# Optimization experiments

Measured on AMD Instinct MI355X. Metric: run time of the kernel, lower is better.

Reference implementation:

```python
import jax, jax.numpy as jnp
import numpy as np

K = 2  # kernel_size


def setup_inputs() -> dict:
    key = jax.random.key(0)
    k1, k2, k3, k4, k5 = jax.random.split(key, 5)
    B, C, H, W_sp = 8, 256, 128, 128
    N = 512                      # number of keypoints
    E = C * K * K                # embed_dim = 1024
    img_feat_highres = jax.random.normal(k1, (B, C, H, W_sp), dtype=jnp.float32)
    W = jax.random.normal(k2, (E, C, K, K), dtype=jnp.float32) * 0.02  # conv weight, OIHW
    b = jax.random.normal(k3, (E,), dtype=jnp.float32) * 0.02          # conv bias
    batch_indices = jnp.broadcast_to(jnp.arange(B, dtype=jnp.int64)[:, None], (B, N))
    pixel_x_id = jax.random.randint(k4, (B, N), 0, H // 2, dtype=jnp.int64)  # low-res ids
    pixel_y_id = jax.random.randint(k5, (B, N), 0, H // 2, dtype=jnp.int64)
    return {
        "img_feat_highres": img_feat_highres,
        "W": W,
        "b": b,
        "batch_indices": batch_indices,
        "pixel_x_id": pixel_x_id,
        "pixel_y_id": pixel_y_id,
    }


def reference(img_feat_highres, W, b, batch_indices, pixel_x_id, pixel_y_id):
    # Dense conv2d, stride 1, padding = K-1 (torch nn.Conv2d semantics)
    patches = jax.lax.conv_general_dilated(
        img_feat_highres, W,
        window_strides=(1, 1),
        padding=((K - 1, K - 1), (K - 1, K - 1)),
        dimension_numbers=("NCHW", "OIHW", "NCHW"),
    ) + b[None, :, None, None]  # (B, E, H+K-1, W+K-1)

    y0 = 2 * pixel_y_id  # (B, N)
    x0 = 2 * pixel_x_id

    def samp(dy, dx):
        # advanced indices at dims 0,2,3 (non-adjacent) -> result (B, N, E)
        return patches[batch_indices, :, y0 + dy, x0 + dx]

    local_feat = jnp.concatenate(
        [samp(0, 0), samp(K, 0), samp(0, K), samp(K, K)], axis=2
    )  # (B, N, 4E)
    return jnp.transpose(local_feat, (0, 2, 1))  # (B, 4E, N)
```

## Files before the change

kernel.cpp:

```cpp
#include <hip/hip_runtime.h>
#include <stdint.h>


typedef __attribute__((ext_vector_type(8))) short bf16x8;
typedef __attribute__((ext_vector_type(4))) float f32x4;

#define GAS(p) ((const __attribute__((address_space(1))) void*)(p))
#define LAS(p) ((__attribute__((address_space(3))) void*)(p))

__device__ __forceinline__ unsigned short f2bf(float f) {
    union { float f; uint32_t u; } x; x.f = f;
    uint32_t u = x.u;
    uint32_t r = (u + 0x7FFFu + ((u >> 16) & 1u)) >> 16;
    return (unsigned short)r;
}

__global__ __launch_bounds__(256)
void prep_kernel(const float* __restrict__ img, const float* __restrict__ Wf,
                 unsigned short* __restrict__ Wq, unsigned short* __restrict__ zp,
                 unsigned short* __restrict__ imgT) {
    __shared__ unsigned short sT[8192];
    const int blk = blockIdx.x;
    const int tid = threadIdx.x;

    if (blk < 512) {
        if (blk == 0 && tid < 32) {
            uint4 z = {0, 0, 0, 0};
            ((uint4*)zp)[tid] = z;
        }
        const int t  = blk * 256 + tid;
        const int et = t >> 15;
        const int r1 = t & 32767;
        const int j  = r1 >> 11;
        const int r2 = r1 & 2047;
        const int h  = r2 >> 10;
        const int r3 = r2 & 1023;
        const int chunk = r3 >> 8;
        const int row   = r3 & 255;
        const int e  = et * 256 + row;
        const int kb = j * 64 + h * 32 + chunk * 8;
        unsigned short v[8];
        #pragma unroll
        for (int kk = 0; kk < 8; ++kk) {
            const int k = kb + kk;
            const int c = k & 255;
            const int p = k >> 8;
            v[kk] = f2bf(Wf[(size_t)e * 1024 + c * 4 + p]);
        }
        *(uint4*)&Wq[(size_t)t * 8] = *(const uint4*)v;
        return;
    }

    const int ib = blk - 512;
    const int cc = ib & 3;
    const int y  = (ib >> 2) & 127;
    const int b  = ib >> 9;
    const int xq = tid & 31;
    const int ch = tid >> 5;
    unsigned int* sU = (unsigned int*)sT;
    const size_t pl = ((size_t)b * 256 + cc * 64) * 16384 + (size_t)y * 128;
    #pragma unroll
    for (int it = 0; it < 4; ++it) {
        const int cp = it * 8 + ch;
        const float4 v0 = *(const float4*)&img[pl + (size_t)(2 * cp)     * 16384 + xq * 4];
        const float4 v1 = *(const float4*)&img[pl + (size_t)(2 * cp + 1) * 16384 + xq * 4];
        const float a0[4] = {v0.x, v0.y, v0.z, v0.w};
        const float a1[4] = {v1.x, v1.y, v1.z, v1.w};
        #pragma unroll
        for (int jj = 0; jj < 4; ++jj) {
            const int x = xq * 4 + jj;
            const unsigned int pk = (unsigned)f2bf(a0[jj]) | ((unsigned)f2bf(a1[jj]) << 16);
            sU[x * 32 + (cp ^ (x & 31))] = pk;
        }
    }
    __syncthreads();
    unsigned short* ob = imgT + (((size_t)b * 128 + y) * 128) * 256 + cc * 64;
    #pragma unroll
    for (int jj = 0; jj < 16; ++jj) {
        const int oo = tid + 256 * jj;
        const int xx = oo >> 5;
        const int c2 = oo & 31;
        const unsigned int pk = sU[xx * 32 + (c2 ^ (xx & 31))];
        *(unsigned int*)&ob[(size_t)xx * 256 + c2 * 2] = pk;
    }
}

__global__ __launch_bounds__(512, 1)
void gemm_kernel(const unsigned short* __restrict__ Wq,
                 const unsigned short* __restrict__ imgT,
                 const unsigned short* __restrict__ zp,
                 const int* __restrict__ bidx,
                 const int* __restrict__ pxid,
                 const int* __restrict__ pyid,
                 const float* __restrict__ bias,
                 float* __restrict__ out)
{
    const int orig = blockIdx.x;
    const int xcd  = orig & 7;
    const int s    = orig >> 3;
    const int gnt  = xcd * 8 + (s >> 2);
    const int et   = s & 3;
    const int e0   = et * 256;
    const int g    = gnt >> 1;
    const int n0   = (gnt & 1) * 256;
    const int b = g >> 2, o = g & 3;

    const int tid  = threadIdx.x;
    const int lane = tid & 63;
    const int wid  = tid >> 6;
    const int wm   = wid >> 2;
    const int wn   = wid & 3;

    __shared__ unsigned short sW[2 * 16384];
    __shared__ unsigned short sA[2 * 16384];

    int ayv[2], axv[2];
    size_t apl[2];
    #pragma unroll
    for (int u = 0; u < 2; ++u) {
        const int row = u * 128 + (tid >> 2);
        const int gi = b * 512 + n0 + row;
        apl[u] = (size_t)bidx[gi] * (128 * 128 * 256);
        ayv[u] = 2 * pyid[gi] - 1 + (o & 1) * 2;
        axv[u] = 2 * pxid[gi] - 1 + (o >> 1) * 2;
    }
    const int aswz = (((tid & 3) ^ ((tid >> 3) & 3))) * 8;
    const unsigned short* wq_base = Wq + (size_t)et * 262144 + tid * 8;

    f32x4 acc[8][4];
    #pragma unroll
    for (int m = 0; m < 8; ++m)
        #pragma unroll
        for (int nf = 0; nf < 4; ++nf) acc[m][nf] = (f32x4){0.f, 0.f, 0.f, 0.f};

    auto stageHalf = [&](int j, int h, int buf) {
        #pragma unroll
        for (int u = 0; u < 2; ++u) {
            const unsigned short* src = wq_base + (size_t)(j * 2 + h) * 8192 + u * 4096;
            __builtin_amdgcn_global_load_lds(GAS(src),
                LAS(&sW[buf * 16384 + h * 8192 + u * 4096 + tid * 8]), 16, 0, 0);
        }
        const int p = j >> 2;
        const int csh = (j & 3) * 64 + h * 32 + aswz;
        #pragma unroll
        for (int u = 0; u < 2; ++u) {
            const int yy = ayv[u] + (p >> 1);
            const int xx = axv[u] + (p & 1);
            const unsigned short* src =
                ((unsigned)yy < 128u && (unsigned)xx < 128u)
                    ? imgT + apl[u] + ((size_t)(yy * 128 + xx)) * 256 + csh
                    : zp + aswz;
            __builtin_amdgcn_global_load_lds(GAS(src),
                LAS(&sA[buf * 16384 + h * 8192 + u * 4096 + tid * 8]), 16, 0, 0);
        }
    };

    stageHalf(0, 0, 0);
    stageHalf(0, 1, 0);

    for (int j = 0; j < 16; ++j) {
        const int buf = j & 1;
        #pragma unroll
        for (int h = 0; h < 2; ++h) {
            if (j == 15 && h == 1) { asm volatile("s_waitcnt vmcnt(0)" ::: "memory"); }
            else                   { asm volatile("s_waitcnt vmcnt(4)" ::: "memory"); }
            __builtin_amdgcn_s_barrier();
            if (j < 15) stageHalf(j + 1, h, buf ^ 1);

            bf16x8 af[8];
            {
                const int chunk = lane >> 4;
                const int rb = wm * 128 + (lane & 15);
                #pragma unroll
                for (int m = 0; m < 8; ++m)
                    af[m] = *(const bf16x8*)&sW[buf * 16384 + h * 8192 + chunk * 2048 + (rb + m * 16) * 8];
            }
            #pragma unroll
            for (int nh = 0; nh < 2; ++nh) {
                bf16x8 bfr[2];
                #pragma unroll
                for (int nn = 0; nn < 2; ++nn) {
                    const int row = wn * 64 + (nh * 2 + nn) * 16 + (lane & 15);
                    const int perm = (lane >> 4) ^ ((row >> 1) & 3);
                    bfr[nn] = *(const bf16x8*)&sA[buf * 16384 + h * 8192 + row * 32 + perm * 8];
                }
                __builtin_amdgcn_s_setprio(1);
                #pragma unroll
                for (int m = 0; m < 8; ++m)
                    #pragma unroll
                    for (int nn = 0; nn < 2; ++nn)
                        acc[m][nh * 2 + nn] = __builtin_amdgcn_mfma_f32_16x16x32_bf16(
                            af[m], bfr[nn], acc[m][nh * 2 + nn], 0, 0, 0);
                __builtin_amdgcn_s_setprio(0);
            }
        }
    }

    #pragma unroll
    for (int m = 0; m < 8; ++m) {
        const int eb = e0 + wm * 128 + m * 16 + (lane >> 4) * 4;
        float bv[4];
        #pragma unroll
        for (int reg = 0; reg < 4; ++reg) bv[reg] = bias[eb + reg];
        #pragma unroll
        for (int nf = 0; nf < 4; ++nf) {
            const int nn = n0 + wn * 64 + nf * 16 + (lane & 15);
            #pragma unroll
            for (int reg = 0; reg < 4; ++reg)
                out[((size_t)g * 1024 + eb + reg) * 512 + nn] = acc[m][nf][reg] + bv[reg];
        }
    }
}

extern "C" void kernel_launch(void* const* d_in, const int* in_sizes, int n_in,
                              void* d_out, int out_size, void* d_ws, size_t ws_size,
                              hipStream_t stream) {
    const float* img  = (const float*)d_in[0];
    const float* Wf   = (const float*)d_in[1];
    const float* bias = (const float*)d_in[2];
    const int*   bidx = (const int*)d_in[3];
    const int*   pxid = (const int*)d_in[4];
    const int*   pyid = (const int*)d_in[5];
    float* out = (float*)d_out;

    unsigned short* Wq   = (unsigned short*)((char*)d_ws + (32u << 20));
    unsigned short* zp   = (unsigned short*)((char*)d_ws + (36u << 20));
    unsigned short* imgT = (unsigned short*)((char*)d_ws + (64u << 20));

    hipLaunchKernelGGL(prep_kernel, dim3(4608), dim3(256), 0, stream,
                       img, Wf, Wq, zp, imgT);
    hipLaunchKernelGGL(gemm_kernel, dim3(256), dim3(512), 0, stream,
                       Wq, imgT, zp, bidx, pxid, pyid, bias, out);
}
```

Measured before the change: 79.67 us.

## Deepen GEMM LDS pipeline to four buffers with three k-tiles in flight

Replaces the two-buffer, half-tile staging with a four-slot ring of 32-wide k-tiles in LDS, prefetching three tiles ahead. The waitcnt thresholds are adjusted so that up to two later stages stay in flight while one is consumed. The aim is to hide the latency of the gathered global-to-LDS loads behind MFMA work. LDS use stays the same (4x8192 per array), and the weight prep layout is re-indexed to match the flat k-tile order.

```diff
diff --git a/kernel.cpp b/kernel.cpp
--- a/kernel.cpp
+++ b/kernel.cpp
@@ -31,14 +31,12 @@
         const int t  = blk * 256 + tid;
         const int et = t >> 15;
         const int r1 = t & 32767;
-        const int j  = r1 >> 11;
-        const int r2 = r1 & 2047;
-        const int h  = r2 >> 10;
-        const int r3 = r2 & 1023;
-        const int chunk = r3 >> 8;
-        const int row   = r3 & 255;
+        const int jt = r1 >> 10;
+        const int r2 = r1 & 1023;
+        const int chunk = r2 >> 8;
+        const int row   = r2 & 255;
         const int e  = et * 256 + row;
-        const int kb = j * 64 + h * 32 + chunk * 8;
+        const int kb = jt * 32 + chunk * 8;
         unsigned short v[8];
         #pragma unroll
         for (int kk = 0; kk < 8; ++kk) {
@@ -111,8 +109,8 @@
     const int wm   = wid >> 2;
     const int wn   = wid & 3;
 
-    __shared__ unsigned short sW[2 * 16384];
-    __shared__ unsigned short sA[2 * 16384];
+    __shared__ unsigned short sW[4][8192];
+    __shared__ unsigned short sA[4][8192];
 
     int ayv[2], axv[2];
     size_t apl[2];
@@ -133,15 +131,13 @@
         #pragma unroll
         for (int nf = 0; nf < 4; ++nf) acc[m][nf] = (f32x4){0.f, 0.f, 0.f, 0.f};
 
-    auto stageHalf = [&](int j, int h, int buf) {
-        #pragma unroll
-        for (int u = 0; u < 2; ++u) {
-            const unsigned short* src = wq_base + (size_t)(j * 2 + h) * 8192 + u * 4096;
-            __builtin_amdgcn_global_load_lds(GAS(src),
-                LAS(&sW[buf * 16384 + h * 8192 + u * 4096 + tid * 8]), 16, 0, 0);
-        }
-        const int p = j >> 2;
-        const int csh = (j & 3) * 64 + h * 32 + aswz;
+    auto stage = [&](int jt, int buf) {
+        #pragma unroll
+        for (int u = 0; u < 2; ++u)
+            __builtin_amdgcn_global_load_lds(GAS(wq_base + (size_t)jt * 8192 + u * 4096),
+                LAS(&sW[buf][u * 4096 + tid * 8]), 16, 0, 0);
+        const int p   = jt >> 3;
+        const int csh = (jt & 7) * 32 + aswz;
         #pragma unroll
         for (int u = 0; u < 2; ++u) {
             const int yy = ayv[u] + (p >> 1);
@@ -151,48 +147,47 @@
                     ? imgT + apl[u] + ((size_t)(yy * 128 + xx)) * 256 + csh
                     : zp + aswz;
             __builtin_amdgcn_global_load_lds(GAS(src),
-                LAS(&sA[buf * 16384 + h * 8192 + u * 4096 + tid * 8]), 16, 0, 0);
+                LAS(&sA[buf][u * 4096 + tid * 8]), 16, 0, 0);
         }
     };
 
-    stageHalf(0, 0, 0);
-    stageHalf(0, 1, 0);
-
-    for (int j = 0; j < 16; ++j) {
-        const int buf = j & 1;
-        #pragma unroll
-        for (int h = 0; h < 2; ++h) {
-            if (j == 15 && h == 1) { asm volatile("s_waitcnt vmcnt(0)" ::: "memory"); }
-            else                   { asm volatile("s_waitcnt vmcnt(4)" ::: "memory"); }
-            __builtin_amdgcn_s_barrier();
-            if (j < 15) stageHalf(j + 1, h, buf ^ 1);
-
-            bf16x8 af[8];
-            {
-                const int chunk = lane >> 4;
-                const int rb = wm * 128 + (lane & 15);
+    stage(0, 0);
+    stage(1, 1);
+    stage(2, 2);
+
+    for (int j = 0; j < 32; ++j) {
+        const int buf = j & 3;
+        if (j < 30)      { asm volatile("s_waitcnt vmcnt(8)" ::: "memory"); }
+        else if (j == 30){ asm volatile("s_waitcnt vmcnt(4)" ::: "memory"); }
+        else             { asm volatile("s_waitcnt vmcnt(0)" ::: "memory"); }
+        __builtin_amdgcn_s_barrier();
+        if (j + 3 < 32) stage(j + 3, (j + 3) & 3);
+
+        bf16x8 af[8];
+        {
+            const int chunk = lane >> 4;
+            const int rb = wm * 128 + (lane & 15);
+            #pragma unroll
+            for (int m = 0; m < 8; ++m)
+                af[m] = *(const bf16x8*)&sW[buf][chunk * 2048 + (rb + m * 16) * 8];
+        }
+        #pragma unroll
+        for (int nh = 0; nh < 2; ++nh) {
+            bf16x8 bfr[2];
+            #pragma unroll
+            for (int nn = 0; nn < 2; ++nn) {
+                const int row = wn * 64 + (nh * 2 + nn) * 16 + (lane & 15);
+                const int perm = (lane >> 4) ^ ((row >> 1) & 3);
+                bfr[nn] = *(const bf16x8*)&sA[buf][row * 32 + perm * 8];
+            }
+            __builtin_amdgcn_s_setprio(1);
+            #pragma unroll
+            for (int m = 0; m < 8; ++m)
                 #pragma unroll
-                for (int m = 0; m < 8; ++m)
-                    af[m] = *(const bf16x8*)&sW[buf * 16384 + h * 8192 + chunk * 2048 + (rb + m * 16) * 8];
-            }
-            #pragma unroll
-            for (int nh = 0; nh < 2; ++nh) {
-                bf16x8 bfr[2];
-                #pragma unroll
-                for (int nn = 0; nn < 2; ++nn) {
-                    const int row = wn * 64 + (nh * 2 + nn) * 16 + (lane & 15);
-                    const int perm = (lane >> 4) ^ ((row >> 1) & 3);
-                    bfr[nn] = *(const bf16x8*)&sA[buf * 16384 + h * 8192 + row * 32 + perm * 8];
-                }
-                __builtin_amdgcn_s_setprio(1);
-                #pragma unroll
-                for (int m = 0; m < 8; ++m)
-                    #pragma unroll
-                    for (int nn = 0; nn < 2; ++nn)
-                        acc[m][nh * 2 + nn] = __builtin_amdgcn_mfma_f32_16x16x32_bf16(
-                            af[m], bfr[nn], acc[m][nh * 2 + nn], 0, 0, 0);
-                __builtin_amdgcn_s_setprio(0);
-            }
+                for (int nn = 0; nn < 2; ++nn)
+                    acc[m][nh * 2 + nn] = __builtin_amdgcn_mfma_f32_16x16x32_bf16(
+                        af[m], bfr[nn], acc[m][nh * 2 + nn], 0, 0, 0);
+            __builtin_amdgcn_s_setprio(0);
         }
     }
 
```

Result: slower. 87.38 us (+9.7%).

## Fuse prep and GEMM kernels into one cooperative launch with grid sync

Applied to the files above, without the earlier changes.

Merges the weight/image conversion kernel and the gather-GEMM kernel into a single cooperative kernel of 256 blocks of 512 threads. Each block converts its share of the weights and transposes 16 image row-chunks to bf16, then waits on a grid-wide sync before running the GEMM. This removes one kernel launch and the gap between the two kernels. In exchange, the prep phase now runs on only 256 blocks at one block per CU with a serial loop, and it pays the cost of a grid barrier.

```diff
diff --git a/kernel.cpp b/kernel.cpp
--- a/kernel.cpp
+++ b/kernel.cpp
@@ -1,5 +1,8 @@
 #include <hip/hip_runtime.h>
+#include <hip/hip_cooperative_groups.h>
 #include <stdint.h>
+
+namespace cg = cooperative_groups;
 
 
 typedef __attribute__((ext_vector_type(8))) short bf16x8;
@@ -15,20 +18,24 @@
     return (unsigned short)r;
 }
 
-__global__ __launch_bounds__(256)
-void prep_kernel(const float* __restrict__ img, const float* __restrict__ Wf,
-                 unsigned short* __restrict__ Wq, unsigned short* __restrict__ zp,
-                 unsigned short* __restrict__ imgT) {
-    __shared__ unsigned short sT[8192];
+__global__ __launch_bounds__(512, 1)
+void fused_kernel(const float* __restrict__ img, const float* __restrict__ Wf,
+                  const float* __restrict__ bias,
+                  const int* __restrict__ bidx, const int* __restrict__ pxid,
+                  const int* __restrict__ pyid,
+                  unsigned short* __restrict__ Wq, unsigned short* __restrict__ zp,
+                  unsigned short* __restrict__ imgT, float* __restrict__ out)
+{
+    __shared__ unsigned short smem[65536];
     const int blk = blockIdx.x;
     const int tid = threadIdx.x;
 
-    if (blk < 512) {
+    {
         if (blk == 0 && tid < 32) {
             uint4 z = {0, 0, 0, 0};
             ((uint4*)zp)[tid] = z;
         }
-        const int t  = blk * 256 + tid;
+        const int t  = blk * 512 + tid;
         const int et = t >> 15;
         const int r1 = t & 32767;
         const int j  = r1 >> 11;
@@ -48,71 +55,66 @@
             v[kk] = f2bf(Wf[(size_t)e * 1024 + c * 4 + p]);
         }
         *(uint4*)&Wq[(size_t)t * 8] = *(const uint4*)v;
-        return;
-    }
-
-    const int ib = blk - 512;
-    const int cc = ib & 3;
-    const int y  = (ib >> 2) & 127;
-    const int b  = ib >> 9;
-    const int xq = tid & 31;
-    const int ch = tid >> 5;
-    unsigned int* sU = (unsigned int*)sT;
-    const size_t pl = ((size_t)b * 256 + cc * 64) * 16384 + (size_t)y * 128;
-    #pragma unroll
-    for (int it = 0; it < 4; ++it) {
-        const int cp = it * 8 + ch;
-        const float4 v0 = *(const float4*)&img[pl + (size_t)(2 * cp)     * 16384 + xq * 4];
-        const float4 v1 = *(const float4*)&img[pl + (size_t)(2 * cp + 1) * 16384 + xq * 4];
-        const float a0[4] = {v0.x, v0.y, v0.z, v0.w};
-        const float a1[4] = {v1.x, v1.y, v1.z, v1.w};
-        #pragma unroll
-        for (int jj = 0; jj < 4; ++jj) {
-            const int x = xq * 4 + jj;
-            const unsigned int pk = (unsigned)f2bf(a0[jj]) | ((unsigned)f2bf(a1[jj]) << 16);
-            sU[x * 32 + (cp ^ (x & 31))] = pk;
-        }
-    }
-    __syncthreads();
-    unsigned short* ob = imgT + (((size_t)b * 128 + y) * 128) * 256 + cc * 64;
-    #pragma unroll
-    for (int jj = 0; jj < 16; ++jj) {
-        const int oo = tid + 256 * jj;
-        const int xx = oo >> 5;
-        const int c2 = oo & 31;
-        const unsigned int pk = sU[xx * 32 + (c2 ^ (xx & 31))];
-        *(unsigned int*)&ob[(size_t)xx * 256 + c2 * 2] = pk;
-    }
-}
-
-__global__ __launch_bounds__(512, 1)
-void gemm_kernel(const unsigned short* __restrict__ Wq,
-                 const unsigned short* __restrict__ imgT,
-                 const unsigned short* __restrict__ zp,
-                 const int* __restrict__ bidx,
-                 const int* __restrict__ pxid,
-                 const int* __restrict__ pyid,
-                 const float* __restrict__ bias,
-                 float* __restrict__ out)
-{
-    const int orig = blockIdx.x;
+
+        const int half = tid >> 8;
+        const int lt   = tid & 255;
+        unsigned int* sU = (unsigned int*)&smem[half * 8192];
+        const int xq = lt & 31;
+        const int ch = lt >> 5;
+        #pragma unroll 1
+        for (int i = 0; i < 8; ++i) {
+            const int u  = blk * 16 + half * 8 + i;
+            const int cc = u & 3;
+            const int y  = (u >> 2) & 127;
+            const int b  = u >> 9;
+            const size_t pl = ((size_t)b * 256 + cc * 64) * 16384 + (size_t)y * 128;
+            #pragma unroll
+            for (int it = 0; it < 4; ++it) {
+                const int cp = it * 8 + ch;
+                const float4 v0 = *(const float4*)&img[pl + (size_t)(2 * cp)     * 16384 + xq * 4];
+                const float4 v1 = *(const float4*)&img[pl + (size_t)(2 * cp + 1) * 16384 + xq * 4];
+                const float a0[4] = {v0.x, v0.y, v0.z, v0.w};
+                const float a1[4] = {v1.x, v1.y, v1.z, v1.w};
+                #pragma unroll
+                for (int jj = 0; jj < 4; ++jj) {
+                    const int x = xq * 4 + jj;
+                    const unsigned int pk = (unsigned)f2bf(a0[jj]) | ((unsigned)f2bf(a1[jj]) << 16);
+                    sU[x * 32 + (cp ^ (x & 31))] = pk;
+                }
+            }
+            __syncthreads();
+            unsigned short* ob = imgT + (((size_t)b * 128 + y) * 128) * 256 + cc * 64;
+            #pragma unroll
+            for (int jj = 0; jj < 16; ++jj) {
+                const int oo = lt + 256 * jj;
+                const int xx = oo >> 5;
+                const int c2 = oo & 31;
+                const unsigned int pk = sU[xx * 32 + (c2 ^ (xx & 31))];
+                *(unsigned int*)&ob[(size_t)xx * 256 + c2 * 2] = pk;
+            }
+            __syncthreads();
+        }
+    }
+
+    cg::this_grid().sync();
+
+    unsigned short* sW = smem;
+    unsigned short* sA = smem + 32768;
+
+    const int orig = blk;
     const int xcd  = orig & 7;
     const int s    = orig >> 3;
     const int gnt  = xcd * 8 + (s >> 2);
-    const int et   = s & 3;
-    const int e0   = et * 256;
+    const int et2  = s & 3;
+    const int e0   = et2 * 256;
     const int g    = gnt >> 1;
     const int n0   = (gnt & 1) * 256;
     const int b = g >> 2, o = g & 3;
 
-    const int tid  = threadIdx.x;
     const int lane = tid & 63;
     const int wid  = tid >> 6;
     const int wm   = wid >> 2;
     const int wn   = wid & 3;
-
-    __shared__ unsigned short sW[2 * 16384];
-    __shared__ unsigned short sA[2 * 16384];
 
     int ayv[2], axv[2];
     size_t apl[2];
@@ -125,7 +127,7 @@
         axv[u] = 2 * pxid[gi] - 1 + (o >> 1) * 2;
     }
     const int aswz = (((tid & 3) ^ ((tid >> 3) & 3))) * 8;
-    const unsigned short* wq_base = Wq + (size_t)et * 262144 + tid * 8;
+    const unsigned short* wq_base = Wq + (size_t)et2 * 262144 + tid * 8;
 
     f32x4 acc[8][4];
     #pragma unroll
@@ -227,8 +229,9 @@
     unsigned short* zp   = (unsigned short*)((char*)d_ws + (36u << 20));
     unsigned short* imgT = (unsigned short*)((char*)d_ws + (64u << 20));
 
-    hipLaunchKernelGGL(prep_kernel, dim3(4608), dim3(256), 0, stream,
-                       img, Wf, Wq, zp, imgT);
-    hipLaunchKernelGGL(gemm_kernel, dim3(256), dim3(512), 0, stream,
-                       Wq, imgT, zp, bidx, pxid, pyid, bias, out);
+    void* args[] = {(void*)&img, (void*)&Wf, (void*)&bias, (void*)&bidx,
+                    (void*)&pxid, (void*)&pyid, (void*)&Wq, (void*)&zp,
+                    (void*)&imgT, (void*)&out};
+    hipLaunchCooperativeKernel((const void*)fused_kernel, dim3(256), dim3(512),
+                               args, 0, stream);
 }
```

After: 128.3 us. 61.1% more time.
